# Performance work log

Measured on AMD Instinct MI355X. Metric: run time of the kernel, lower is better.

## Reference

```python
import jax, jax.numpy as jnp
import numpy as np

MAX_CAV = 5


def setup_inputs() -> dict:
    key = jax.random.key(0)
    k1, k2, k3, k4, k5 = jax.random.split(key, 5)
    # ragged group lengths, each <= MAX_CAV, sum = 25
    record_len = jnp.array([3, 5, 2, 4, 1, 5, 3, 2], dtype=jnp.int32)
    N, C, H, W = 25, 256, 48, 176
    x = jax.random.normal(k1, (N, C, H, W), dtype=jnp.float32)
    W1 = jax.random.normal(k2, (MAX_CAV, 2 * MAX_CAV), dtype=jnp.float32) * 0.3
    W2 = jax.random.normal(k3, (MAX_CAV, MAX_CAV), dtype=jnp.float32) * 0.3
    conv_w = jax.random.normal(k4, (MAX_CAV,), dtype=jnp.float32) * 0.3
    conv_b = jax.random.normal(k5, (1,), dtype=jnp.float32) * 0.1
    return dict(x=x, record_len=record_len, W1=W1, W2=W2, conv_w=conv_w, conv_b=conv_b)


def _pad_regroup(x, record_len, max_cav):
    # scatter ragged tokens into a zero-padded [bs, max_cav, C, H, W] buffer
    N = x.shape[0]
    bs = record_len.shape[0]
    cum = jnp.cumsum(record_len)
    tok = jnp.arange(N)
    b = jnp.searchsorted(cum, tok, side='right')      # batch id per token
    slot = tok - (cum[b] - record_len[b])             # position within group
    padded = jnp.zeros((bs, max_cav) + x.shape[1:], x.dtype)
    return padded.at[b, slot].set(x)


def reference(x, record_len, W1, W2, conv_w, conv_b):
    padded = _pad_regroup(x, record_len, MAX_CAV)     # [bs, M, C, H, W]
    # AdaptiveAvg/MaxPool3d(1) over (C,H,W); padded slots are all-zero -> max=0
    x_avg = padded.mean(axis=(2, 3, 4))               # [bs, M]
    x_max = padded.max(axis=(2, 3, 4))                # [bs, M]
    x_sq = jnp.concatenate([x_avg, x_max], axis=1)    # [bs, 2M]
    gate = jax.nn.relu(jax.nn.sigmoid(x_sq @ W1.T) @ W2.T)  # [bs, M]
    scaled = padded * gate[:, :, None, None, None]
    # 1x1x1 Conv3d(M -> 1) == weighted sum over CAV axis + bias, then ReLU
    out = jax.nn.relu(jnp.einsum('m,bmchw->bchw', conv_w, scaled) + conv_b[0])
    return out
```

## Files before the change

### kernel.cpp

```cpp
#include <hip/hip_runtime.h>
#include <math.h>

#define CHW     2162688
#define V4      540672
#define NTOK    25
#define MAXCAV  5
#define NBATCH  8

#define BPT     64
#define V4_BLK  8448
#define ITERS   33

#define ABLKS   2048
#define CHUNK3  264

typedef float f32x4 __attribute__((ext_vector_type(4)));

__global__ __launch_bounds__(256) void k_reduce(const float4* __restrict__ x,
                                                float* __restrict__ psum,
                                                float* __restrict__ pmax) {
    const int tid = threadIdx.x;
    const int t   = blockIdx.y;
    const int blk = blockIdx.x;
    const long base = (long)t * V4 + (long)blk * V4_BLK;

    float s = 0.0f;
    float mx = -INFINITY;
    #pragma unroll 4
    for (int i = 0; i < ITERS; ++i) {
        float4 v = x[base + i * 256 + tid];
        s += (v.x + v.y) + (v.z + v.w);
        mx = fmaxf(mx, fmaxf(fmaxf(v.x, v.y), fmaxf(v.z, v.w)));
    }

    const int lane = tid & 63;
    const int wave = tid >> 6;
    #pragma unroll
    for (int off = 32; off > 0; off >>= 1) {
        s += __shfl_xor(s, off, 64);
        mx = fmaxf(mx, __shfl_xor(mx, off, 64));
    }
    __shared__ float rs[4], rm[4];
    if (lane == 0) { rs[wave] = s; rm[wave] = mx; }
    __syncthreads();
    if (tid == 0) {
        psum[t * BPT + blk] = rs[0] + rs[1] + rs[2] + rs[3];
        pmax[t * BPT + blk] = fmaxf(fmaxf(rm[0], rm[1]), fmaxf(rm[2], rm[3]));
    }
}

__global__ __launch_bounds__(256) void k_gate(const float* __restrict__ psum,
                                              const float* __restrict__ pmax,
                                              const int*   __restrict__ record_len,
                                              const float* __restrict__ W1,
                                              const float* __restrict__ W2,
                                              const float* __restrict__ conv_w,
                                              int*   __restrict__ starts,
                                              float* __restrict__ coefs) {
    __shared__ float tsum[NTOK], tmax[NTOK];
    const int wave = threadIdx.x >> 6;
    const int lane = threadIdx.x & 63;

    for (int t = wave; t < NTOK; t += 4) {
        float s = psum[t * BPT + lane];
        float m = pmax[t * BPT + lane];
        #pragma unroll
        for (int off = 32; off > 0; off >>= 1) {
            s += __shfl_xor(s, off, 64);
            m = fmaxf(m, __shfl_xor(m, off, 64));
        }
        if (lane == 0) { tsum[t] = s; tmax[t] = m; }
    }
    __syncthreads();

    if ((int)threadIdx.x < NBATCH) {
        const int b = threadIdx.x;
        int start = 0;
        for (int i = 0; i < b; ++i) start += record_len[i];
        const int len = record_len[b];
        starts[b] = start;

        float xsq[2 * MAXCAV];
        #pragma unroll
        for (int m = 0; m < MAXCAV; ++m) {
            const bool valid = m < len;
            xsq[m]          = valid ? tsum[start + m] * (1.0f / (float)CHW) : 0.0f;
            xsq[MAXCAV + m] = valid ? tmax[start + m] : 0.0f;
        }
        float h[MAXCAV];
        #pragma unroll
        for (int j = 0; j < MAXCAV; ++j) {
            float a = 0.0f;
            #pragma unroll
            for (int k = 0; k < 2 * MAXCAV; ++k) a += xsq[k] * W1[j * 2 * MAXCAV + k];
            h[j] = 1.0f / (1.0f + expf(-a));
        }
        #pragma unroll
        for (int m = 0; m < MAXCAV; ++m) {
            float g = 0.0f;
            #pragma unroll
            for (int j = 0; j < MAXCAV; ++j) g += h[j] * W2[m * MAXCAV + j];
            coefs[b * MAXCAV + m] = conv_w[m] * fmaxf(g, 0.0f);
        }
    }
}

__device__ __forceinline__ void relu_store(float ax, float ay, float az, float aw,
                                           float4* __restrict__ out, int o) {
    f32x4 acc;
    acc.x = fmaxf(ax, 0.0f);
    acc.y = fmaxf(ay, 0.0f);
    acc.z = fmaxf(az, 0.0f);
    acc.w = fmaxf(aw, 0.0f);
    __builtin_nontemporal_store(acc, (f32x4*)(out + o));
}

template <int LEN>
__device__ __forceinline__ void apply_idx(const float4* __restrict__ x,
                                          const float* c, float bias,
                                          int start, int obase, int idx,
                                          float4* __restrict__ out) {
    float ax = bias, ay = bias, az = bias, aw = bias;
    #pragma unroll
    for (int m = 0; m < LEN; ++m) {
        float4 v = x[(start + m) * V4 + idx];
        ax += c[m] * v.x;
        ay += c[m] * v.y;
        az += c[m] * v.z;
        aw += c[m] * v.w;
    }
    relu_store(ax, ay, az, aw, out, obase + idx);
}

template <int LEN>
__device__ __forceinline__ void apply_chunk(const float4* __restrict__ x,
                                            const float* c, float bias,
                                            int start, int obase, int base3,
                                            int tid, float4* __restrict__ out) {
    apply_idx<LEN>(x, c, bias, start, obase, base3 + tid, out);
    if (tid < CHUNK3 - 256)
        apply_idx<LEN>(x, c, bias, start, obase, base3 + 256 + tid, out);
}

__global__ __launch_bounds__(256) void k_apply(const float4* __restrict__ x,
                                               const int*   __restrict__ record_len,
                                               const int*   __restrict__ starts,
                                               const float* __restrict__ coefs,
                                               const float* __restrict__ conv_b,
                                               float4* __restrict__ out) {
    const int tid   = threadIdx.x;
    const int base3 = blockIdx.x * CHUNK3;
    const float bias = conv_b[0];

    for (int b = 0; b < NBATCH; ++b) {
        const int len   = record_len[b];
        const int start = starts[b];
        float c[MAXCAV];
        #pragma unroll
        for (int m = 0; m < MAXCAV; ++m) c[m] = coefs[b * MAXCAV + m];
        const int obase = b * V4;

        switch (len) {
            case 1:  apply_chunk<1>(x, c, bias, start, obase, base3, tid, out); break;
            case 2:  apply_chunk<2>(x, c, bias, start, obase, base3, tid, out); break;
            case 3:  apply_chunk<3>(x, c, bias, start, obase, base3, tid, out); break;
            case 4:  apply_chunk<4>(x, c, bias, start, obase, base3, tid, out); break;
            default: apply_chunk<5>(x, c, bias, start, obase, base3, tid, out); break;
        }
    }
}

extern "C" void kernel_launch(void* const* d_in, const int* in_sizes, int n_in,
                              void* d_out, int out_size, void* d_ws, size_t ws_size,
                              hipStream_t stream) {
    const float4* x  = (const float4*)d_in[0];
    const int*    rl = (const int*)d_in[1];
    const float*  W1 = (const float*)d_in[2];
    const float*  W2 = (const float*)d_in[3];
    const float*  cw = (const float*)d_in[4];
    const float*  cb = (const float*)d_in[5];
    float4* out = (float4*)d_out;

    char* ws = (char*)d_ws;
    float* psum   = (float*)(ws);
    float* pmax   = (float*)(ws + 6400);
    int*   starts = (int*)  (ws + 12800);
    float* coefs  = (float*)(ws + 12864);

    k_reduce<<<dim3(BPT, NTOK), 256, 0, stream>>>(x, psum, pmax);
    k_gate<<<1, 256, 0, stream>>>(psum, pmax, rl, W1, W2, cw, starts, coefs);
    k_apply<<<ABLKS, 256, 0, stream>>>(x, rl, starts, coefs, cb, out);
}
```

Before: 88.09 us.

## Flatten apply loop over tokens with per-token coefficients and group-end stores

The gate kernel now emits a per-token coefficient and a per-token group-end marker, so the apply kernel walks all 25 tokens in one unrolled loop instead of switching on group length per batch. Each thread handles two float4 elements, 512 per block, with fewer blocks, giving a uniform branch-light loop with many independent loads in flight. Stores happen at each group end and the accumulator is reset. The catch is higher register pressure from the 25 cached coefficients and markers, and a per-token branch.

```diff
diff --git a/kernel.cpp b/kernel.cpp
--- a/kernel.cpp
+++ b/kernel.cpp
@@ -11,8 +11,8 @@
 #define V4_BLK  8448
 #define ITERS   33
 
-#define ABLKS   2048
-#define CHUNK3  264
+#define ABLKS   1056
+#define CHUNK3  512
 
 typedef float f32x4 __attribute__((ext_vector_type(4)));
 
@@ -55,11 +55,15 @@
                                               const float* __restrict__ W1,
                                               const float* __restrict__ W2,
                                               const float* __restrict__ conv_w,
-                                              int*   __restrict__ starts,
-                                              float* __restrict__ coefs) {
+                                              float* __restrict__ tok_coef,
+                                              int*   __restrict__ tok_end)
+{
     __shared__ float tsum[NTOK], tmax[NTOK];
+    __shared__ float scoef[NBATCH][MAXCAV];
+    __shared__ int   sstart[NBATCH], slen[NBATCH];
     const int wave = threadIdx.x >> 6;
     const int lane = threadIdx.x & 63;
+    const int tid  = threadIdx.x;
 
     for (int t = wave; t < NTOK; t += 4) {
         float s = psum[t * BPT + lane];
@@ -73,12 +77,13 @@
     }
     __syncthreads();
 
-    if ((int)threadIdx.x < NBATCH) {
-        const int b = threadIdx.x;
+    if (tid < NBATCH) {
+        const int b = tid;
         int start = 0;
         for (int i = 0; i < b; ++i) start += record_len[i];
         const int len = record_len[b];
-        starts[b] = start;
+        sstart[b] = start;
+        slen[b]   = len;
 
         float xsq[2 * MAXCAV];
         #pragma unroll
@@ -100,72 +105,62 @@
             float g = 0.0f;
             #pragma unroll
             for (int j = 0; j < MAXCAV; ++j) g += h[j] * W2[m * MAXCAV + j];
-            coefs[b * MAXCAV + m] = conv_w[m] * fmaxf(g, 0.0f);
+            scoef[b][m] = conv_w[m] * fmaxf(g, 0.0f);
         }
+    }
+    __syncthreads();
+
+    if (tid < NTOK) {
+        int b = 0;
+        #pragma unroll
+        for (int i = 0; i < NBATCH; ++i)
+            if (tid >= sstart[i] + slen[i]) b = i + 1;
+        const int m = tid - sstart[b];
+        tok_coef[tid] = scoef[b][m];
+        tok_end[tid]  = (m == slen[b] - 1) ? b : -1;
     }
 }
 
-__device__ __forceinline__ void relu_store(float ax, float ay, float az, float aw,
-                                           float4* __restrict__ out, int o) {
+__device__ __forceinline__ void relu_store(f32x4 a, float4* __restrict__ out, int o) {
     f32x4 acc;
-    acc.x = fmaxf(ax, 0.0f);
-    acc.y = fmaxf(ay, 0.0f);
-    acc.z = fmaxf(az, 0.0f);
-    acc.w = fmaxf(aw, 0.0f);
+    acc.x = fmaxf(a.x, 0.0f);
+    acc.y = fmaxf(a.y, 0.0f);
+    acc.z = fmaxf(a.z, 0.0f);
+    acc.w = fmaxf(a.w, 0.0f);
     __builtin_nontemporal_store(acc, (f32x4*)(out + o));
 }
 
-template <int LEN>
-__device__ __forceinline__ void apply_idx(const float4* __restrict__ x,
-                                          const float* c, float bias,
-                                          int start, int obase, int idx,
-                                          float4* __restrict__ out) {
-    float ax = bias, ay = bias, az = bias, aw = bias;
-    #pragma unroll
-    for (int m = 0; m < LEN; ++m) {
-        float4 v = x[(start + m) * V4 + idx];
-        ax += c[m] * v.x;
-        ay += c[m] * v.y;
-        az += c[m] * v.z;
-        aw += c[m] * v.w;
-    }
-    relu_store(ax, ay, az, aw, out, obase + idx);
-}
-
-template <int LEN>
-__device__ __forceinline__ void apply_chunk(const float4* __restrict__ x,
-                                            const float* c, float bias,
-                                            int start, int obase, int base3,
-                                            int tid, float4* __restrict__ out) {
-    apply_idx<LEN>(x, c, bias, start, obase, base3 + tid, out);
-    if (tid < CHUNK3 - 256)
-        apply_idx<LEN>(x, c, bias, start, obase, base3 + 256 + tid, out);
-}
-
 __global__ __launch_bounds__(256) void k_apply(const float4* __restrict__ x,
-                                               const int*   __restrict__ record_len,
-                                               const int*   __restrict__ starts,
-                                               const float* __restrict__ coefs,
+                                               const float* __restrict__ tok_coef,
+                                               const int*   __restrict__ tok_end,
                                                const float* __restrict__ conv_b,
                                                float4* __restrict__ out) {
-    const int tid   = threadIdx.x;
-    const int base3 = blockIdx.x * CHUNK3;
+    const int tid = threadIdx.x;
+    const int idx = blockIdx.x * CHUNK3 + tid;
     const float bias = conv_b[0];
 
-    for (int b = 0; b < NBATCH; ++b) {
-        const int len   = record_len[b];
-        const int start = starts[b];
-        float c[MAXCAV];
-        #pragma unroll
-        for (int m = 0; m < MAXCAV; ++m) c[m] = coefs[b * MAXCAV + m];
-        const int obase = b * V4;
+    float tc[NTOK];
+    int   te[NTOK];
+    #pragma unroll
+    for (int t = 0; t < NTOK; ++t) { tc[t] = tok_coef[t]; te[t] = tok_end[t]; }
 
-        switch (len) {
-            case 1:  apply_chunk<1>(x, c, bias, start, obase, base3, tid, out); break;
-            case 2:  apply_chunk<2>(x, c, bias, start, obase, base3, tid, out); break;
-            case 3:  apply_chunk<3>(x, c, bias, start, obase, base3, tid, out); break;
-            case 4:  apply_chunk<4>(x, c, bias, start, obase, base3, tid, out); break;
-            default: apply_chunk<5>(x, c, bias, start, obase, base3, tid, out); break;
+    f32x4 a0, a1;
+    a0.x = a0.y = a0.z = a0.w = bias;
+    a1 = a0;
+
+    #pragma unroll
+    for (int t = 0; t < NTOK; ++t) {
+        const float4 v0 = x[t * V4 + idx];
+        const float4 v1 = x[t * V4 + idx + 256];
+        const float c = tc[t];
+        a0.x += c * v0.x;  a0.y += c * v0.y;  a0.z += c * v0.z;  a0.w += c * v0.w;
+        a1.x += c * v1.x;  a1.y += c * v1.y;  a1.z += c * v1.z;  a1.w += c * v1.w;
+        if (te[t] >= 0) {
+            const int obase = te[t] * V4 + idx;
+            relu_store(a0, out, obase);
+            relu_store(a1, out, obase + 256);
+            a0.x = a0.y = a0.z = a0.w = bias;
+            a1 = a0;
         }
     }
 }
@@ -182,12 +177,12 @@
     float4* out = (float4*)d_out;
 
     char* ws = (char*)d_ws;
-    float* psum   = (float*)(ws);
-    float* pmax   = (float*)(ws + 6400);
-    int*   starts = (int*)  (ws + 12800);
-    float* coefs  = (float*)(ws + 12864);
+    float* psum     = (float*)(ws);
+    float* pmax     = (float*)(ws + 6400);
+    float* tok_coef = (float*)(ws + 12800);
+    int*   tok_end  = (int*)  (ws + 12800 + 128);
 
     k_reduce<<<dim3(BPT, NTOK), 256, 0, stream>>>(x, psum, pmax);
-    k_gate<<<1, 256, 0, stream>>>(psum, pmax, rl, W1, W2, cw, starts, coefs);
-    k_apply<<<ABLKS, 256, 0, stream>>>(x, rl, starts, coefs, cb, out);
+    k_gate<<<1, 256, 0, stream>>>(psum, pmax, rl, W1, W2, cw, tok_coef, tok_end);
+    k_apply<<<ABLKS, 256, 0, stream>>>(x, tok_coef, tok_end, cb, out);
 }
```

After: 82.36 us, median of 2. 1.07x faster.
